# Kernel tuning notes

Measured on AMD Instinct MI355X. Metric: run time of the kernel, lower is better.

## Reference

```python
import jax, jax.numpy as jnp
import numpy as np

NUM_HEADS = 32  # head_dim = input_dim // num_heads = 32 == C (forced by matmul contraction)


def setup_inputs() -> dict:
    key = jax.random.key(0)
    ks = jax.random.split(key, 8)
    B, C, D3, H1 = 16, 32, 1, 32
    input_dim = 1024  # == C**2, forced by the final view(B, C, H1, W1)
    s = 0.02
    x1 = jax.random.normal(ks[0], (B, C, D3, H1, input_dim), jnp.float32)
    x2 = jax.random.normal(ks[1], (B, C, D3, H1, input_dim), jnp.float32)
    Wq = jax.random.normal(ks[2], (input_dim, input_dim), jnp.float32) * s
    bq = jax.random.normal(ks[3], (input_dim,), jnp.float32) * s
    Wk = jax.random.normal(ks[4], (input_dim, input_dim), jnp.float32) * s
    bk = jax.random.normal(ks[5], (input_dim,), jnp.float32) * s
    Wv = jax.random.normal(ks[6], (input_dim, input_dim), jnp.float32) * s
    bv = jax.random.normal(ks[7], (input_dim,), jnp.float32) * s
    return {"x1": x1, "x2": x2, "Wq": Wq, "bq": bq, "Wk": Wk, "bk": bk, "Wv": Wv, "bv": bv}


def reference(x1, x2, Wq, bq, Wk, bk, Wv, bv):
    B, C, _, H1, W1 = x1.shape  # W1 == input_dim (Linear acts on last dim)
    nh = NUM_HEADS
    hd = W1 // nh
    # Linear projections on the last axis (torch Linear: x @ W.T + b)
    q = (x1 @ Wq.T + bq).reshape(B, C, nh, hd, -1).transpose(0, 2, 4, 3, 1)  # (B, nh, L1, hd, C)
    k = (x2 @ Wk.T + bk).reshape(B, C, nh, hd, -1)                            # (B, C, nh, hd, L2)
    v = (x2 @ Wv.T + bv).reshape(B, C, nh, hd, -1)                            # (B, C, nh, hd, L2)
    # Broadcasted batched matmul: contracts q's trailing C axis with k's hd axis (C == hd).
    energy = jnp.matmul(q, k)                      # (B, C, L1, hd, L2)
    attention = jax.nn.softmax(energy, axis=-1)    # softmax over L2
    # Contracts v's L2 axis with attention's hd axis (L2 == hd).
    out = jnp.matmul(v, attention)                 # (B, C, L1, hd, L2)
    out = out.transpose(0, 2, 4, 3, 1).reshape(B, C, H1, W1)
    return out
```

## Files before the change

kernel.cpp:

```cpp
#include <hip/hip_runtime.h>
#include <cstdint>

typedef __bf16 bf16x8 __attribute__((ext_vector_type(8)));
typedef float f32x4 __attribute__((ext_vector_type(4)));
typedef unsigned short us8 __attribute__((ext_vector_type(8)));

__device__ __forceinline__ unsigned short f2bf(float f) {
  union { float f; uint32_t u; } c; c.f = f;
  uint32_t u = c.u + 0x7FFFu + ((c.u >> 16) & 1u);
  return (unsigned short)(u >> 16);
}
__device__ __forceinline__ float bf2f(unsigned short u) {
  union { uint32_t u; float f; } c; c.u = ((uint32_t)u) << 16; return c.f;
}

__global__ __launch_bounds__(256) void cvt5(
    const float* __restrict__ x1, const float* __restrict__ x2,
    const float* __restrict__ Wq, const float* __restrict__ Wk, const float* __restrict__ Wv,
    unsigned short* __restrict__ xb1, unsigned short* __restrict__ xb2,
    unsigned short* __restrict__ wb) {
  int z = blockIdx.y;
  const float* src; unsigned short* dst; int n4;
  if (z == 0)      { src = x1; dst = xb1;            n4 = 16777216 / 4; }
  else if (z == 1) { src = x2; dst = xb2;            n4 = 16777216 / 4; }
  else if (z == 2) { src = Wq; dst = wb;             n4 = 1048576 / 4; }
  else if (z == 3) { src = Wk; dst = wb + 1048576;   n4 = 1048576 / 4; }
  else             { src = Wv; dst = wb + 2*1048576; n4 = 1048576 / 4; }
  for (int i = blockIdx.x * 256 + threadIdx.x; i < n4; i += gridDim.x * 256) {
    float4 v = ((const float4*)src)[i];
    ushort4 o;
    o.x = f2bf(v.x); o.y = f2bf(v.y); o.z = f2bf(v.z); o.w = f2bf(v.w);
    ((ushort4*)dst)[i] = o;
  }
}

__global__ __launch_bounds__(512) void gemm_qkv(
    const unsigned short* __restrict__ xb1, const unsigned short* __restrict__ xb2,
    const unsigned short* __restrict__ wb,
    const float* __restrict__ bq, const float* __restrict__ bk, const float* __restrict__ bv,
    unsigned short* __restrict__ qkv) {
  __shared__ __attribute__((aligned(16))) unsigned short sm[65536];
  unsigned short* lA0 = sm;
  unsigned short* lB0 = sm + 16384;
  unsigned short* lA1 = sm + 32768;
  unsigned short* lB1 = sm + 49152;

  const int id = blockIdx.x;
  const int swz = (id & 7) * 96 + (id >> 3);
  const int z = swz >> 8;
  const int rem = swz & 255;
  const int mb = rem >> 2;
  const int nb = rem & 3;
  const int m0 = mb * 256;
  const int n0 = nb * 256;

  const unsigned short* Ag = (z == 0) ? xb1 : xb2;
  const unsigned short* Wg = wb + z * 1048576;
  const float* bias = (z == 0) ? bq : (z == 1 ? bk : bv);
  unsigned short* C = qkv + z * 16777216;

  const int tid = threadIdx.x;
  const int lane = tid & 63;
  const int wv = tid >> 6;
  const int wm = wv >> 2;
  const int wn = wv & 3;
  const int mr = lane & 15;
  const int quad = lane >> 4;

  const int rl = lane >> 3;
  const int cg = (lane & 7) ^ rl;

  const unsigned short* aptr[4];
  const unsigned short* bptr[4];
  int ldoff[4];
#pragma unroll
  for (int half = 0; half < 2; ++half)
#pragma unroll
    for (int ld = 0; ld < 2; ++ld) {
      const int q2 = half * 2 + ld;
      const int chunk = wv * 2 + ld;
      const int rt = half * 128 + chunk * 8 + rl;
      aptr[q2] = Ag + (m0 + rt) * 1024 + cg * 8;
      const int wrow = (z == 1) ? ((rt & 31) * 32 + nb * 8 + (rt >> 5)) : (n0 + rt);
      bptr[q2] = Wg + wrow * 1024 + cg * 8;
      ldoff[q2] = half * 8192 + chunk * 512;
    }

  const int sg0 = ((quad) ^ (mr & 7)) * 8;
  const int sg1 = ((4 + quad) ^ (mr & 7)) * 8;
  const int arow = (wm * 128 + mr) * 64;
  const int brow = (wn * 64 + mr) * 64;

  f32x4 acc[8][4];
#pragma unroll
  for (int i = 0; i < 8; ++i)
#pragma unroll
    for (int j = 0; j < 4; ++j) acc[i][j] = (f32x4){0.f, 0.f, 0.f, 0.f};

  bf16x8 af[4][2], bfr[4][2];

  auto STA = [&](unsigned short* dst, int kt) {
#pragma unroll
    for (int q2 = 0; q2 < 4; ++q2)
      __builtin_amdgcn_global_load_lds(
          (const __attribute__((address_space(1))) void*)(aptr[q2] + kt * 64),
          (__attribute__((address_space(3))) void*)(dst + ldoff[q2]), 16, 0, 0);
  };
  auto STB = [&](unsigned short* dst, int kt) {
#pragma unroll
    for (int q2 = 0; q2 < 4; ++q2)
      __builtin_amdgcn_global_load_lds(
          (const __attribute__((address_space(1))) void*)(bptr[q2] + kt * 64),
          (__attribute__((address_space(3))) void*)(dst + ldoff[q2]), 16, 0, 0);
  };
  auto RDA = [&](const unsigned short* lA, int ib) {
#pragma unroll
    for (int i = 0; i < 4; ++i) {
      af[i][0] = *(const bf16x8*)(lA + arow + (ib + i) * 1024 + sg0);
      af[i][1] = *(const bf16x8*)(lA + arow + (ib + i) * 1024 + sg1);
    }
  };
  auto RDB = [&](const unsigned short* lB, int jb) {
#pragma unroll
    for (int j = 0; j < 2; ++j) {
      bfr[jb + j][0] = *(const bf16x8*)(lB + brow + (jb + j) * 1024 + sg0);
      bfr[jb + j][1] = *(const bf16x8*)(lB + brow + (jb + j) * 1024 + sg1);
    }
  };
  auto MF = [&](int ib, int jb) {
#pragma unroll
    for (int i = 0; i < 4; ++i)
#pragma unroll
      for (int j = 0; j < 2; ++j)
#pragma unroll
        for (int h = 0; h < 2; ++h)
          acc[ib + i][jb + j] = __builtin_amdgcn_mfma_f32_16x16x32_bf16(
              af[i][h], bfr[jb + j][h], acc[ib + i][jb + j], 0, 0, 0);
  };

  STA(lA0, 0);
  STB(lB0, 0);
  STA(lA1, 1);
  asm volatile("s_waitcnt vmcnt(4)" ::: "memory");
  __builtin_amdgcn_s_barrier();

#pragma unroll 1
  for (int t = 0; t < 8; ++t) {
    const bool lastt = (t == 7);
    RDA(lA0, 0); RDB(lB0, 0);
    STB(lB1, 2 * t + 1);
    __builtin_amdgcn_s_barrier();
    __builtin_amdgcn_s_setprio(1); MF(0, 0); __builtin_amdgcn_s_setprio(0);
    __builtin_amdgcn_s_barrier();
    RDB(lB0, 2);
    __builtin_amdgcn_s_barrier();
    __builtin_amdgcn_s_setprio(1); MF(0, 2); __builtin_amdgcn_s_setprio(0);
    __builtin_amdgcn_s_barrier();
    RDA(lA0, 4);
    __builtin_amdgcn_s_barrier();
    __builtin_amdgcn_s_setprio(1); MF(4, 0); __builtin_amdgcn_s_setprio(0);
    __builtin_amdgcn_s_barrier();
    if (!lastt) STA(lA0, 2 * t + 2);
    __builtin_amdgcn_s_barrier();
    __builtin_amdgcn_s_setprio(1); MF(4, 2); __builtin_amdgcn_s_setprio(0);
    if (lastt) { asm volatile("s_waitcnt vmcnt(0)" ::: "memory"); }
    else       { asm volatile("s_waitcnt vmcnt(4)" ::: "memory"); }
    __builtin_amdgcn_s_barrier();
    RDA(lA1, 0); RDB(lB1, 0);
    if (!lastt) STB(lB0, 2 * t + 2);
    __builtin_amdgcn_s_barrier();
    __builtin_amdgcn_s_setprio(1); MF(0, 0); __builtin_amdgcn_s_setprio(0);
    __builtin_amdgcn_s_barrier();
    RDB(lB1, 2);
    __builtin_amdgcn_s_barrier();
    __builtin_amdgcn_s_setprio(1); MF(0, 2); __builtin_amdgcn_s_setprio(0);
    __builtin_amdgcn_s_barrier();
    RDA(lA1, 4);
    __builtin_amdgcn_s_barrier();
    __builtin_amdgcn_s_setprio(1); MF(4, 0); __builtin_amdgcn_s_setprio(0);
    __builtin_amdgcn_s_barrier();
    if (!lastt) STA(lA1, 2 * t + 3);
    __builtin_amdgcn_s_barrier();
    __builtin_amdgcn_s_setprio(1); MF(4, 2); __builtin_amdgcn_s_setprio(0);
    if (!lastt) { asm volatile("s_waitcnt vmcnt(4)" ::: "memory"); }
    __builtin_amdgcn_s_barrier();
  }

  {
    unsigned short* strip = sm + wv * 8192;
    float bb[4];
#pragma unroll
    for (int j = 0; j < 4; ++j) {
      int colp = n0 + wn * 64 + j * 16 + mr;
      int col = (z == 1) ? ((colp & 31) * 32 + (colp >> 5)) : colp;
      bb[j] = bias[col];
    }
#pragma unroll
    for (int i = 0; i < 8; ++i)
#pragma unroll
      for (int j = 0; j < 4; ++j)
#pragma unroll
        for (int r = 0; r < 4; ++r) {
          int row = i * 16 + quad * 4 + r;
          int byteoff = (row * 128 + j * 32 + mr * 2) ^ (((row >> 2) & 3) << 5);
          *(unsigned short*)((char*)strip + byteoff) = f2bf(acc[i][j][r] + bb[j]);
        }
    const int r8 = lane >> 3, c8 = lane & 7;
#pragma unroll
    for (int it = 0; it < 16; ++it) {
      int row = it * 8 + r8;
      int byteoff = (row * 128 + c8 * 16) ^ (((row >> 2) & 3) << 5);
      uint4 vv = *(const uint4*)((const char*)strip + byteoff);
      *(uint4*)(C + (m0 + wm * 128 + row) * 1024 + n0 + wn * 64 + c8 * 8) = vv;
    }
  }
}

__global__ __launch_bounds__(256) void attn(const unsigned short* __restrict__ qkv,
                                            unsigned short* __restrict__ obuf) {
  const unsigned short* qbuf = qkv;
  const unsigned short* kbuf = qkv + 16777216;
  const unsigned short* vbuf = qkv + 2 * 16777216;
  __shared__ __attribute__((aligned(16))) unsigned short qs[8192];
  __shared__ __attribute__((aligned(16))) unsigned short ats[4][1280];
  __shared__ __attribute__((aligned(16))) unsigned short obb[4][1024];
  const int id = blockIdx.x;
  const int xcd = id & 7;
  const int pos = id >> 3;
  const int y0 = (pos & 3) * 8;
  const int bx = (pos >> 2) * 8 + xcd;
  const int b = bx >> 5;
  const int x = bx & 31;
  const int lane = threadIdx.x & 63;
  const int wv = threadIdx.x >> 6;
  const int mr = lane & 15, quad = lane >> 4;

  uint4 kpre[2][2], vpre[2][2];
#pragma unroll
  for (int s = 0; s < 2; ++s) {
    int y = y0 + wv * 2 + s;
    const unsigned short* krow = kbuf + ((b * 32 + x) * 32 + y) * 1024;
    const unsigned short* vrow = vbuf + ((b * 32 + x) * 32 + y) * 1024;
#pragma unroll
    for (int lt = 0; lt < 2; ++lt)
      kpre[s][lt] = *(const uint4*)(krow + (lt * 16 + mr) * 32 + quad * 8);
#pragma unroll
    for (int i = 0; i < 2; ++i)
      vpre[s][i] = *(const uint4*)(vrow + (i * 16 + mr) * 32 + quad * 8);
  }

#pragma unroll
  for (int it = 0; it < 4; ++it) {
    int cl = threadIdx.x + 256 * it;
    int t = cl >> 5, m = cl & 31;
    uint4 v = *(const uint4*)(qbuf + ((b * 1024 + t * 32 + x) * 1024 + m * 32 + y0));
    us8 e = __builtin_bit_cast(us8, v);
    int g = ((t >> 3) ^ ((m >> 1) & 3)) * 8 + (t & 7);
#pragma unroll
    for (int dy = 0; dy < 8; ++dy)
      qs[dy * 1024 + m * 32 + g] = e[dy];
  }
  __syncthreads();

  for (int s = 0; s < 2; ++s) {
    int y = y0 + wv * 2 + s;
    int dy = wv * 2 + s;

    bf16x8 qa[2], kb[2];
#pragma unroll
    for (int mt = 0; mt < 2; ++mt)
      qa[mt] = *(const bf16x8*)(qs + dy * 1024 + (mt * 16 + mr) * 32 +
                                (quad ^ ((mr >> 1) & 3)) * 8);
    kb[0] = __builtin_bit_cast(bf16x8, kpre[s][0]);
    kb[1] = __builtin_bit_cast(bf16x8, kpre[s][1]);

    f32x4 e[2][2];
#pragma unroll
    for (int mt = 0; mt < 2; ++mt)
#pragma unroll
      for (int lt = 0; lt < 2; ++lt) {
        f32x4 zz = (f32x4){0.f, 0.f, 0.f, 0.f};
        e[mt][lt] = __builtin_amdgcn_mfma_f32_16x16x32_bf16(qa[mt], kb[lt], zz, 0, 0, 0);
      }

#pragma unroll
    for (int mt = 0; mt < 2; ++mt)
#pragma unroll
      for (int r = 0; r < 4; ++r) {
        float v0 = e[mt][0][r], v1 = e[mt][1][r];
        float mx = fmaxf(v0, v1);
#pragma unroll
        for (int off = 1; off < 16; off <<= 1) mx = fmaxf(mx, __shfl_xor(mx, off));
        float p0 = __expf(v0 - mx), p1 = __expf(v1 - mx);
        float sm = p0 + p1;
#pragma unroll
        for (int off = 1; off < 16; off <<= 1) sm += __shfl_xor(sm, off);
        float inv = 1.0f / sm;
        p0 *= inv; p1 *= inv;
        int trow = mt * 16 + quad * 4 + r;
        ats[wv][mr * 40 + trow] = f2bf(p0);
        ats[wv][(16 + mr) * 40 + trow] = f2bf(p1);
      }

    bf16x8 va[2], pb[2];
    va[0] = __builtin_bit_cast(bf16x8, vpre[s][0]);
    va[1] = __builtin_bit_cast(bf16x8, vpre[s][1]);
#pragma unroll
    for (int lt = 0; lt < 2; ++lt)
      pb[lt] = *(const bf16x8*)(&ats[wv][(lt * 16 + mr) * 40 + quad * 8]);
    f32x4 o[2][2];
#pragma unroll
    for (int i = 0; i < 2; ++i)
#pragma unroll
      for (int lt = 0; lt < 2; ++lt) {
        f32x4 zz = (f32x4){0.f, 0.f, 0.f, 0.f};
        o[i][lt] = __builtin_amdgcn_mfma_f32_16x16x32_bf16(va[i], pb[lt], zz, 0, 0, 0);
      }

#pragma unroll
    for (int i = 0; i < 2; ++i)
#pragma unroll
      for (int lt = 0; lt < 2; ++lt)
#pragma unroll
        for (int r = 0; r < 4; ++r)
          obb[wv][(i * 16 + quad * 4 + r) * 32 + lt * 16 + mr] = f2bf(o[i][lt][r]);
    unsigned short* orow = obuf + ((b * 32 + x) * 32 + y) * 1024;
#pragma unroll
    for (int h = 0; h < 2; ++h)
      *(uint4*)(orow + h * 512 + lane * 8) = *(const uint4*)(&obb[wv][h * 512 + lane * 8]);
  }
}

__global__ __launch_bounds__(256) void transpose2(const unsigned short* __restrict__ obuf,
                                                  float* __restrict__ out) {
  __shared__ float t[2][32][36];
  const int y = blockIdx.y, b = blockIdx.z;
  const int r = threadIdx.x >> 3;
  const int cg = threadIdx.x & 7;
  for (int mi = 0; mi < 8; ++mi) {
    int m = blockIdx.x * 8 + mi;
    int buf = mi & 1;
    ushort4 v = *(const ushort4*)(obuf + ((b * 32 + r) * 32 + y) * 1024 + m * 32 + cg * 4);
    t[buf][r][cg * 4 + 0] = bf2f(v.x);
    t[buf][r][cg * 4 + 1] = bf2f(v.y);
    t[buf][r][cg * 4 + 2] = bf2f(v.z);
    t[buf][r][cg * 4 + 3] = bf2f(v.w);
    __syncthreads();
    float4 w;
    w.x = t[buf][cg * 4 + 0][r];
    w.y = t[buf][cg * 4 + 1][r];
    w.z = t[buf][cg * 4 + 2][r];
    w.w = t[buf][cg * 4 + 3][r];
    *(float4*)(out + ((b * 32 + y) * 32 + r) * 1024 + m * 32 + cg * 4) = w;
  }
}

extern "C" void kernel_launch(void* const* d_in, const int* in_sizes, int n_in,
                              void* d_out, int out_size, void* d_ws, size_t ws_size,
                              hipStream_t stream) {
  const float* x1 = (const float*)d_in[0];
  const float* x2 = (const float*)d_in[1];
  const float* Wq = (const float*)d_in[2];
  const float* bq = (const float*)d_in[3];
  const float* Wk = (const float*)d_in[4];
  const float* bk = (const float*)d_in[5];
  const float* Wv = (const float*)d_in[6];
  const float* bv = (const float*)d_in[7];
  float* out = (float*)d_out;

  char* ws = (char*)d_ws;
  unsigned short* xb1 = (unsigned short*)ws;
  unsigned short* xb2 = xb1 + 16777216;
  unsigned short* wb = xb2 + 16777216;
  unsigned short* qkv = wb + 3 * 1048576;
  unsigned short* obuf16 = (unsigned short*)ws;

  cvt5<<<dim3(2048, 5), 256, 0, stream>>>(x1, x2, Wq, Wk, Wv, xb1, xb2, wb);
  gemm_qkv<<<dim3(768), 512, 0, stream>>>(xb1, xb2, wb, bq, bk, bv, qkv);
  attn<<<dim3(2048), 256, 0, stream>>>(qkv, obuf16);
  transpose2<<<dim3(4, 32, 16), 256, 0, stream>>>(obuf16, out);
}
```

Baseline: 324.9 us.

## Write Q projection in attention-ready transposed layout from GEMM epilogue

The GEMM epilogue for the Q projection (z==0) now writes its output in a transposed layout through shared memory, so that the attention kernel can load Q rows directly with vector loads like K and V. This removes the attention kernel's strided Q gather, its shared-memory transpose and a block barrier. In exchange the GEMM epilogue adds a __syncthreads and scalar 16-bit shared reads gathered across two wave strips.

```diff
diff --git a/kernel.cpp b/kernel.cpp
--- a/kernel.cpp
+++ b/kernel.cpp
@@ -205,13 +205,38 @@
           int byteoff = (row * 128 + j * 32 + mr * 2) ^ (((row >> 2) & 3) << 5);
           *(unsigned short*)((char*)strip + byteoff) = f2bf(acc[i][j][r] + bb[j]);
         }
-    const int r8 = lane >> 3, c8 = lane & 7;
-#pragma unroll
-    for (int it = 0; it < 16; ++it) {
-      int row = it * 8 + r8;
-      int byteoff = (row * 128 + c8 * 16) ^ (((row >> 2) & 3) << 5);
-      uint4 vv = *(const uint4*)((const char*)strip + byteoff);
-      *(uint4*)(C + (m0 + wm * 128 + row) * 1024 + n0 + wn * 64 + c8 * 8) = vv;
+    if (z == 0) {
+      __syncthreads();
+      const int bq = mb >> 2;
+      const int t0 = (mb & 3) * 8;
+      const int cT = (lane & 1) * 32 + (lane >> 1);
+      const int m_ = nb * 8 + wn * 2 + (cT >> 5);
+      const int y_ = cT & 31;
+      const unsigned short* s0 = sm + wn * 8192;
+      const unsigned short* s1 = sm + (4 + wn) * 8192;
+#pragma unroll
+      for (int it = 0; it < 16; ++it) {
+        const int x_ = it * 2 + wm;
+        const int sw = ((x_ >> 2) & 3) << 5;
+        us8 pk;
+#pragma unroll
+        for (int tau = 0; tau < 8; ++tau) {
+          const unsigned short* sb = (tau >> 2) ? s1 : s0;
+          int byteoff = (((tau & 3) * 32 + x_) * 128 + cT * 2) ^ sw;
+          pk[tau] = *(const unsigned short*)((const char*)sb + byteoff);
+        }
+        *(uint4*)(C + bq * 1048576 + x_ * 32768 + y_ * 1024 + m_ * 32 + t0) =
+            __builtin_bit_cast(uint4, pk);
+      }
+    } else {
+      const int r8 = lane >> 3, c8 = lane & 7;
+#pragma unroll
+      for (int it = 0; it < 16; ++it) {
+        int row = it * 8 + r8;
+        int byteoff = (row * 128 + c8 * 16) ^ (((row >> 2) & 3) << 5);
+        uint4 vv = *(const uint4*)((const char*)strip + byteoff);
+        *(uint4*)(C + (m0 + wm * 128 + row) * 1024 + n0 + wn * 64 + c8 * 8) = vv;
+      }
     }
   }
 }
@@ -221,7 +246,6 @@
   const unsigned short* qbuf = qkv;
   const unsigned short* kbuf = qkv + 16777216;
   const unsigned short* vbuf = qkv + 2 * 16777216;
-  __shared__ __attribute__((aligned(16))) unsigned short qs[8192];
   __shared__ __attribute__((aligned(16))) unsigned short ats[4][1280];
   __shared__ __attribute__((aligned(16))) unsigned short obb[4][1024];
   const int id = blockIdx.x;
@@ -235,12 +259,17 @@
   const int wv = threadIdx.x >> 6;
   const int mr = lane & 15, quad = lane >> 4;
 
-  uint4 kpre[2][2], vpre[2][2];
+  uint4 qpre[2][2], kpre[2][2], vpre[2][2];
 #pragma unroll
   for (int s = 0; s < 2; ++s) {
-    int y = y0 + wv * 2 + s;
-    const unsigned short* krow = kbuf + ((b * 32 + x) * 32 + y) * 1024;
-    const unsigned short* vrow = vbuf + ((b * 32 + x) * 32 + y) * 1024;
+    const int y = y0 + wv * 2 + s;
+    const int rowbase = ((b * 32 + x) * 32 + y) * 1024;
+    const unsigned short* qrow = qbuf + rowbase;
+    const unsigned short* krow = kbuf + rowbase;
+    const unsigned short* vrow = vbuf + rowbase;
+#pragma unroll
+    for (int mt = 0; mt < 2; ++mt)
+      qpre[s][mt] = *(const uint4*)(qrow + (mt * 16 + mr) * 32 + quad * 8);
 #pragma unroll
     for (int lt = 0; lt < 2; ++lt)
       kpre[s][lt] = *(const uint4*)(krow + (lt * 16 + mr) * 32 + quad * 8);
@@ -249,28 +278,12 @@
       vpre[s][i] = *(const uint4*)(vrow + (i * 16 + mr) * 32 + quad * 8);
   }
 
-#pragma unroll
-  for (int it = 0; it < 4; ++it) {
-    int cl = threadIdx.x + 256 * it;
-    int t = cl >> 5, m = cl & 31;
-    uint4 v = *(const uint4*)(qbuf + ((b * 1024 + t * 32 + x) * 1024 + m * 32 + y0));
-    us8 e = __builtin_bit_cast(us8, v);
-    int g = ((t >> 3) ^ ((m >> 1) & 3)) * 8 + (t & 7);
-#pragma unroll
-    for (int dy = 0; dy < 8; ++dy)
-      qs[dy * 1024 + m * 32 + g] = e[dy];
-  }
-  __syncthreads();
-
   for (int s = 0; s < 2; ++s) {
-    int y = y0 + wv * 2 + s;
-    int dy = wv * 2 + s;
+    const int y = y0 + wv * 2 + s;
 
     bf16x8 qa[2], kb[2];
-#pragma unroll
-    for (int mt = 0; mt < 2; ++mt)
-      qa[mt] = *(const bf16x8*)(qs + dy * 1024 + (mt * 16 + mr) * 32 +
-                                (quad ^ ((mr >> 1) & 3)) * 8);
+    qa[0] = __builtin_bit_cast(bf16x8, qpre[s][0]);
+    qa[1] = __builtin_bit_cast(bf16x8, qpre[s][1]);
     kb[0] = __builtin_bit_cast(bf16x8, kpre[s][0]);
     kb[1] = __builtin_bit_cast(bf16x8, kpre[s][1]);
 
```

After: 342.8 us. +5.5%, slower.
